# Kernel optimization log

Hardware: AMD Instinct MI355X
Metric: run time of the kernel (lower is better)

Reference implementation:

```python
import jax, jax.numpy as jnp
import numpy as np

NUM_BITS = 16           # continuousVarEncodingNumBits
THRESH = 4.0            # segmentActivationThreshold
K_SYN = 32              # numberOfSynapsesPerSegment
B, F, H, C = 512, 128, 8192, 10
E = F * NUM_BITS        # encodedFeatureSize = 2048


def _make_weight(key, n, p):
    # Dense int8-style weights: ~K_SYN random +/-1 synapses per neuron, rest 0.
    k1, k2 = jax.random.split(key)
    signs = jnp.where(jax.random.bernoulli(k1, 0.5, (n, p)), 1.0, -1.0)
    mask = jax.random.bernoulli(k2, K_SYN / p, (n, p))
    return (signs * mask).astype(jnp.float32)


def setup_inputs() -> dict:
    key = jax.random.key(0)
    ks = jax.random.split(key, 6)
    x = jax.random.uniform(ks[0], (B, F), dtype=jnp.float32)
    W0 = _make_weight(ks[1], H, E)   # layer 0: hidden x encoded
    W1 = _make_weight(ks[2], H, H)
    W2 = _make_weight(ks[3], H, H)
    # output connection matrix (numberOfHiddenLayers, hidden, classes); float variant
    outConn = jax.random.uniform(ks[4], (3, H, C), dtype=jnp.float32)
    return {"trainOrTest": 0, "x": x, "W0": W0, "W1": W1, "W2": W2, "outConn": outConn}


def reference(trainOrTest, x, W0, W1, W2, outConn):
    # thermometer bit-encoding of continuous vars: bit j on if x*NUM_BITS > j
    levels = jnp.arange(NUM_BITS, dtype=x.dtype)
    bits = jnp.where(x[:, :, None] * NUM_BITS > levels, 1.0, 0.0)  # (B, F, NUM_BITS)
    act = bits.reshape(x.shape[0], -1).astype(jnp.float32)          # (B, E)

    outAct = jnp.zeros((x.shape[0], outConn.shape[-1]), dtype=jnp.float32)
    for i, W in enumerate((W0, W1, W2)):
        z = act @ W.T                                   # segment sums (B, H)
        act = jnp.where(z >= THRESH, 1.0, 0.0)          # binary segment activation
        outAct = outAct + jnp.einsum('bh,hc->bc', act, outConn[i])
    preds = jnp.argmax(outAct, axis=-1)
    return preds, outAct
```

## Files before the change

### kernel.cpp

```cpp
#include <hip/hip_runtime.h>
#include <stdint.h>

#define BATCH   512
#define NFEAT   128
#define ESIZE   2048
#define HSIZE   8192
#define NCLS    10
#define THRESH_I 4
#define CAP     128
#define ROWB    64

typedef float vf4 __attribute__((ext_vector_type(4)));


__global__ __launch_bounds__(256) void encode_kernel(
    const float* __restrict__ x,
    uint8_t* __restrict__ aT0, uint8_t* __restrict__ aT1,
    uint8_t* __restrict__ aT2, uint8_t* __restrict__ aT3,
    int* __restrict__ counts,
    float* __restrict__ outAcc) {
  int t = blockIdx.x * 256 + threadIdx.x;
  if (t < BATCH * NCLS) outAcc[t] = 0.0f;
  else if (t < 5120 + 64)  aT0[(size_t)ESIZE * ROWB + (t - 5120)] = 0;
  else if (t < 5184 + 64)  aT1[(size_t)HSIZE * ROWB + (t - 5184)] = 0;
  else if (t < 5248 + 64)  aT2[(size_t)HSIZE * ROWB + (t - 5248)] = 0;
  else if (t < 5312 + 64)  aT3[(size_t)HSIZE * ROWB + (t - 5312)] = 0;
  counts[t] = 0;
  counts[t + 8192] = 0;
  counts[t + 16384] = 0;

  int wave = threadIdx.x >> 6;
  int lane = threadIdx.x & 63;
  int f = blockIdx.x * 4 + wave;
  if (f < NFEAT) {
    float u[8];
#pragma unroll
    for (int i = 0; i < 8; ++i)
      u[i] = x[(size_t)(lane + 64 * i) * NFEAT + f] * 16.0f;
#pragma unroll
    for (int j = 0; j < 16; ++j) {
      uint32_t byte = 0;
#pragma unroll
      for (int i = 0; i < 8; ++i)
        byte |= (u[i] > (float)j ? 1u : 0u) << i;
      aT0[(size_t)(f * 16 + j) * ROWB + lane] = (uint8_t)byte;
    }
  }
}

__device__ __forceinline__ void cvt_group(
    const vf4* c, int gbase, int ebase, int wid, int lane, uint64_t lmask,
    uint32_t* __restrict__ lists, int* __restrict__ counts) {
  float v[16] = {c[0].x, c[0].y, c[0].z, c[0].w, c[1].x, c[1].y, c[1].z,
                 c[1].w, c[2].x, c[2].y, c[2].z, c[2].w, c[3].x, c[3].y,
                 c[3].z, c[3].w};
  uint64_t m[16];
  int tt[16];
#pragma unroll
  for (int k = 0; k < 16; ++k) {
    m[k] = __ballot(v[k] != 0.0f);
    tt[k] = (int)__popcll(m[k]);
  }
  int total = 0;
#pragma unroll
  for (int k = 0; k < 16; ++k) total += tt[k];
  if (total == 0) return;

  int base = 0;
  if (lane == 0) base = atomicAdd(&counts[wid], total);
  base = __shfl(base, 0);

  uint32_t* lp = lists + (size_t)wid * CAP;
  int off = base;
#pragma unroll
  for (int k = 0; k < 16; ++k) {
    if (v[k] != 0.0f) {
      int pos = off + (int)__popcll(m[k] & lmask);
      int e = ebase + gbase + (k >> 2) * 256 + (k & 3) + lane * 4;
      if (pos < CAP)
        lp[pos] = ((uint32_t)e << 1) | (v[k] < 0.0f ? 1u : 0u);
    }
    off += tt[k];
  }
}

__global__ __launch_bounds__(256, 8) void convert_kernel(
    const float* __restrict__ W0, const float* __restrict__ W1,
    const float* __restrict__ W2,
    uint32_t* __restrict__ lists, int* __restrict__ counts) {
  int unit = (blockIdx.x * 256 + threadIdx.x) >> 6;
  int lane = threadIdx.x & 63;

  const float* W;
  int row, ebase, wid, P;
  if (unit < 8192) {
    W = W0; P = ESIZE; row = unit; ebase = 0; wid = unit;
  } else if (unit < 8192 + 32768) {
    W = W1; P = HSIZE;
    int q = unit - 8192;
    row = q >> 2; ebase = (q & 3) * 2048; wid = HSIZE + row;
  } else {
    W = W2; P = HSIZE;
    int q = unit - 8192 - 32768;
    row = q >> 2; ebase = (q & 3) * 2048; wid = 2 * HSIZE + row;
  }

  const vf4* w4 = (const vf4*)(W + (size_t)row * P + (size_t)ebase);
  vf4 c[8];
#pragma unroll
  for (int j = 0; j < 8; ++j)
    c[j] = __builtin_nontemporal_load(w4 + j * 64 + lane);

  uint64_t lmask = (lane == 0) ? 0ull : (~0ull >> (64 - lane));
  cvt_group(c,     0,    ebase, wid, lane, lmask, lists, counts);
  cvt_group(c + 4, 1024, ebase, wid, lane, lmask, lists, counts);
}

__device__ __forceinline__ void proc_ent(uint32_t ent,
                                         const uint8_t* __restrict__ aIn,
                                         int lane, int* z) {
  uint32_t negm = (uint32_t)(-(int)(ent & 1u));
  uint32_t ee = ent >> 1;
  uint32_t byte = (uint32_t)aIn[(size_t)ee * ROWB + lane];
#pragma unroll
  for (int i = 0; i < 8; ++i) {
    uint32_t t = (byte >> i) & 1u;
    z[i] += (int)((t ^ negm) - negm);
  }
}

__device__ __forceinline__ void proc_comp_dense(float v, int ebase,
                                                const uint8_t* __restrict__ aIn,
                                                int lane, int* z) {
  uint64_t m = __ballot(v != 0.0f);
  if (m == 0ull) return;
  uint64_t pm = __ballot(v > 0.0f);
  do {
    uint32_t src = (uint32_t)__builtin_ctzll(m);
    m &= m - 1;
    int e = ebase + 4 * (int)src;
    uint32_t negm = ((pm >> src) & 1ull) ? 0u : 0xFFFFFFFFu;
    uint32_t byte = (uint32_t)aIn[(size_t)e * ROWB + lane];
#pragma unroll
    for (int i = 0; i < 8; ++i) {
      uint32_t t = (byte >> i) & 1u;
      z[i] += (int)((t ^ negm) - negm);
    }
  } while (m);
}

template <int P>
__global__ __launch_bounds__(512, 4) void layer_kernel(
    const uint32_t* __restrict__ lists, const int* __restrict__ counts,
    const float* __restrict__ W,
    const uint8_t* __restrict__ aIn, uint8_t* __restrict__ aOut) {
  int wave = threadIdx.x >> 6;
  int lane = threadIdx.x & 63;
  int hbase = blockIdx.x * 16 + wave * 2;
  const uint32_t SENT = (uint32_t)(P << 1);

  for (int r = 0; r < 2; ++r) {
    int h = hbase + r;
    int z[8];
#pragma unroll
    for (int i = 0; i < 8; ++i) z[i] = 0;

    int cnt = counts[h];
    if (cnt <= CAP) {
      const uint32_t* lp = lists + (size_t)h * CAP;
      int full = cnt & ~7;
      for (int i = 0; i < full; i += 8) {
        uint4 eA = *(const uint4*)(lp + i);
        uint4 eB = *(const uint4*)(lp + i + 4);
        proc_ent(eA.x, aIn, lane, z);
        proc_ent(eA.y, aIn, lane, z);
        proc_ent(eA.z, aIn, lane, z);
        proc_ent(eA.w, aIn, lane, z);
        proc_ent(eB.x, aIn, lane, z);
        proc_ent(eB.y, aIn, lane, z);
        proc_ent(eB.z, aIn, lane, z);
        proc_ent(eB.w, aIn, lane, z);
      }
      if (cnt & 7) {
        uint4 eA = *(const uint4*)(lp + full);
        uint4 eB = *(const uint4*)(lp + full + 4);
        uint32_t ee[8] = {eA.x, eA.y, eA.z, eA.w, eB.x, eB.y, eB.z, eB.w};
#pragma unroll
        for (int j = 0; j < 8; ++j)
          ee[j] = (full + j < cnt) ? ee[j] : SENT;
#pragma unroll
        for (int j = 0; j < 8; ++j) proc_ent(ee[j], aIn, lane, z);
      }
    } else {
      const float4* wrow = (const float4*)(W + (size_t)h * P) + lane;
      for (int it = 0; it < P / 256; ++it) {
        float4 wv = wrow[it * 64];
        int eb = it * 256;
        proc_comp_dense(wv.x, eb + 0, aIn, lane, z);
        proc_comp_dense(wv.y, eb + 1, aIn, lane, z);
        proc_comp_dense(wv.z, eb + 2, aIn, lane, z);
        proc_comp_dense(wv.w, eb + 3, aIn, lane, z);
      }
    }

    uint32_t ob = 0;
#pragma unroll
    for (int i = 0; i < 8; ++i)
      ob |= (z[i] >= THRESH_I ? 1u : 0u) << i;
    aOut[(size_t)h * ROWB + lane] = (uint8_t)ob;
  }
}

#define OCHUNK 128
__global__ __launch_bounds__(256, 4) void outacc_kernel(
    const float* __restrict__ outConn,
    const uint8_t* __restrict__ a1, const uint8_t* __restrict__ a2,
    const uint8_t* __restrict__ a3,
    float* __restrict__ outAcc) {
  __shared__ float shOC[OCHUNK][NCLS];
  __shared__ float shAcc[BATCH * NCLS];
  int tid = threadIdx.x;
  int gbase = blockIdx.x * OCHUNK;
  for (int idx = tid; idx < OCHUNK * NCLS; idx += 256)
    ((float*)shOC)[idx] = outConn[(size_t)gbase * NCLS + idx];
  for (int idx = tid; idx < BATCH * NCLS; idx += 256) shAcc[idx] = 0.0f;
  __syncthreads();

  int wave = tid >> 6;
  int lane = tid & 63;
  int layer = gbase >> 13;
  const uint8_t* aT = (layer == 0) ? a1 : (layer == 1) ? a2 : a3;
  int h0 = (gbase & (HSIZE - 1)) + wave * 32;

  float acc[8][NCLS];
#pragma unroll
  for (int i = 0; i < 8; ++i)
#pragma unroll
    for (int c = 0; c < NCLS; ++c) acc[i][c] = 0.0f;

  for (int r = 0; r < 32; ++r) {
    int row = h0 + r;
    uint32_t byte = (uint32_t)aT[(size_t)row * ROWB + lane];
    float bf[8];
#pragma unroll
    for (int i = 0; i < 8; ++i) bf[i] = (float)((byte >> i) & 1u);
    const float* oc = shOC[wave * 32 + r];
#pragma unroll
    for (int c = 0; c < NCLS; ++c) {
      float o = oc[c];
#pragma unroll
      for (int i = 0; i < 8; ++i) acc[i][c] += bf[i] * o;
    }
  }
#pragma unroll
  for (int i = 0; i < 8; ++i)
#pragma unroll
    for (int c = 0; c < NCLS; ++c)
      atomicAdd(&shAcc[(size_t)(lane + 64 * i) * NCLS + c], acc[i][c]);
  __syncthreads();
  for (int idx = tid; idx < BATCH * NCLS; idx += 256)
    atomicAdd(&outAcc[idx], shAcc[idx]);
}

__global__ __launch_bounds__(256) void final_kernel(
    const float* __restrict__ outAcc,
    int* __restrict__ preds,
    float* __restrict__ outF) {
  int b = blockIdx.x * 256 + threadIdx.x;
  if (b < BATCH) {
    float vals[NCLS];
#pragma unroll
    for (int c = 0; c < NCLS; ++c) vals[c] = outAcc[b * NCLS + c];
    float best = vals[0];
    int bi = 0;
#pragma unroll
    for (int c = 1; c < NCLS; ++c) {
      if (vals[c] > best) { best = vals[c]; bi = c; }
    }
    preds[b] = bi;
#pragma unroll
    for (int c = 0; c < NCLS; ++c) outF[b * NCLS + c] = vals[c];
  }
}

extern "C" void kernel_launch(void* const* d_in, const int* in_sizes, int n_in,
                              void* d_out, int out_size, void* d_ws, size_t ws_size,
                              hipStream_t stream) {
  const float* x       = (const float*)d_in[1];
  const float* W0      = (const float*)d_in[2];
  const float* W1      = (const float*)d_in[3];
  const float* W2      = (const float*)d_in[4];
  const float* outConn = (const float*)d_in[5];

  uint8_t* base = (uint8_t*)d_ws;
  uint8_t* aT0 = base;
  uint8_t* aT1 = base + 0x40000;
  uint8_t* aT2 = aT1 + 0x90000;
  uint8_t* aT3 = aT2 + 0x90000;
  uint32_t* lists = (uint32_t*)(aT3 + 0x90000);
  int* counts = (int*)((uint8_t*)lists +
                       ((size_t)3 * HSIZE * CAP + 64) * 4);
  float* outAcc = (float*)(counts + 3 * HSIZE);

  encode_kernel<<<32, 256, 0, stream>>>(x, aT0, aT1, aT2, aT3, counts, outAcc);
  convert_kernel<<<18432, 256, 0, stream>>>(W0, W1, W2, lists, counts);
  layer_kernel<ESIZE><<<512, 512, 0, stream>>>(
      lists, counts, W0, aT0, aT1);
  layer_kernel<HSIZE><<<512, 512, 0, stream>>>(
      lists + (size_t)HSIZE * CAP, counts + HSIZE, W1, aT1, aT2);
  layer_kernel<HSIZE><<<512, 512, 0, stream>>>(
      lists + (size_t)2 * HSIZE * CAP, counts + 2 * HSIZE, W2, aT2, aT3);
  outacc_kernel<<<192, 256, 0, stream>>>(outConn, aT1, aT2, aT3, outAcc);
  final_kernel<<<2, 256, 0, stream>>>(outAcc, (int*)d_out,
                                      (float*)d_out + BATCH);
}
```

Before: 627.3 us.

## Fuse layer-0 sparse matvec into weight-conversion kernel, drop layer-0 launch

For W0 rows, the convert kernel now uses ballots over the loaded weights to find the nonzero synapses and accumulates segment sums straight from the bit-packed encoded activations. It thresholds the result and writes the layer-1 input, so building the sparse list and launching a separate layer-0 kernel are no longer needed. This removes one launch and the list write/read round trip for layer 0. The cost is a serialized per-nonzero loop inside each wave of the conversion kernel, which lengthens those waves.

```diff
diff --git a/kernel.cpp b/kernel.cpp
--- a/kernel.cpp
+++ b/kernel.cpp
@@ -84,28 +84,74 @@
   }
 }
 
+__device__ __forceinline__ void fused_group(
+    const vf4* c, int gbase, const uint8_t* __restrict__ aT0,
+    int lane, int* z) {
+  float v[16] = {c[0].x, c[0].y, c[0].z, c[0].w, c[1].x, c[1].y, c[1].z,
+                 c[1].w, c[2].x, c[2].y, c[2].z, c[2].w, c[3].x, c[3].y,
+                 c[3].z, c[3].w};
+#pragma unroll
+  for (int k = 0; k < 16; ++k) {
+    uint64_t m = __ballot(v[k] != 0.0f);
+    if (m == 0ull) continue;
+    uint64_t pm = __ballot(v[k] > 0.0f);
+    int ebase = gbase + (k >> 2) * 256 + (k & 3);
+    do {
+      uint32_t src = (uint32_t)__builtin_ctzll(m);
+      m &= m - 1;
+      int e = ebase + 4 * (int)src;
+      uint32_t negm = ((pm >> src) & 1ull) ? 0u : 0xFFFFFFFFu;
+      uint32_t byte = (uint32_t)aT0[(size_t)e * ROWB + lane];
+#pragma unroll
+      for (int i = 0; i < 8; ++i) {
+        uint32_t t = (byte >> i) & 1u;
+        z[i] += (int)((t ^ negm) - negm);
+      }
+    } while (m);
+  }
+}
+
 __global__ __launch_bounds__(256, 8) void convert_kernel(
     const float* __restrict__ W0, const float* __restrict__ W1,
     const float* __restrict__ W2,
+    const uint8_t* __restrict__ aT0, uint8_t* __restrict__ aT1,
     uint32_t* __restrict__ lists, int* __restrict__ counts) {
   int unit = (blockIdx.x * 256 + threadIdx.x) >> 6;
   int lane = threadIdx.x & 63;
 
+  if (unit < 8192) {
+    int row = unit;
+    const vf4* w4 = (const vf4*)(W0 + (size_t)row * (size_t)ESIZE);
+    vf4 c[8];
+#pragma unroll
+    for (int j = 0; j < 8; ++j)
+      c[j] = __builtin_nontemporal_load(w4 + j * 64 + lane);
+    int z[8];
+#pragma unroll
+    for (int i = 0; i < 8; ++i) z[i] = 0;
+    fused_group(c,     0,    aT0, lane, z);
+    fused_group(c + 4, 1024, aT0, lane, z);
+    uint32_t ob = 0;
+#pragma unroll
+    for (int i = 0; i < 8; ++i)
+      ob |= (z[i] >= THRESH_I ? 1u : 0u) << i;
+    aT1[(size_t)row * ROWB + lane] = (uint8_t)ob;
+    return;
+  }
+
   const float* W;
-  int row, ebase, wid, P;
-  if (unit < 8192) {
-    W = W0; P = ESIZE; row = unit; ebase = 0; wid = unit;
-  } else if (unit < 8192 + 32768) {
-    W = W1; P = HSIZE;
+  int row, ebase, wid;
+  if (unit < 8192 + 32768) {
+    W = W1;
     int q = unit - 8192;
     row = q >> 2; ebase = (q & 3) * 2048; wid = HSIZE + row;
   } else {
-    W = W2; P = HSIZE;
+    W = W2;
     int q = unit - 8192 - 32768;
     row = q >> 2; ebase = (q & 3) * 2048; wid = 2 * HSIZE + row;
   }
 
-  const vf4* w4 = (const vf4*)(W + (size_t)row * P + (size_t)ebase);
+  const vf4* w4 = (const vf4*)(W + (size_t)row * HSIZE + (size_t)ebase);
   vf4 c[8];
 #pragma unroll
   for (int j = 0; j < 8; ++j)
@@ -303,9 +349,7 @@
   float* outAcc = (float*)(counts + 3 * HSIZE);
 
   encode_kernel<<<32, 256, 0, stream>>>(x, aT0, aT1, aT2, aT3, counts, outAcc);
-  convert_kernel<<<18432, 256, 0, stream>>>(W0, W1, W2, lists, counts);
-  layer_kernel<ESIZE><<<512, 512, 0, stream>>>(
-      lists, counts, W0, aT0, aT1);
+  convert_kernel<<<18432, 256, 0, stream>>>(W0, W1, W2, aT0, aT1, lists, counts);
   layer_kernel<HSIZE><<<512, 512, 0, stream>>>(
       lists + (size_t)HSIZE * CAP, counts + HSIZE, W1, aT1, aT2);
   layer_kernel<HSIZE><<<512, 512, 0, stream>>>(
```

After: 614.2 us. -2.1%, faster.
